# Optimization experiments

Hardware: AMD Instinct MI355X
Metric: run time of the kernel (lower is better)

The kernel has to match this reference:

```python
import jax, jax.numpy as jnp
import numpy as np

PAST = 15        # sum(num_classes[:-1])
NC = 20          # sum(num_classes)
ALPHA = 0.99
IGNORE = 255


def setup_inputs() -> dict:
    key = jax.random.key(0)
    k1, k2, k3, k4, k5, k6 = jax.random.split(key, 6)
    B, C, H, W = 8, NC, 512, 512
    logit = jax.random.normal(k1, (B, C, H, W), dtype=jnp.float32)
    # ema_prob is used as probabilities (gathered & compared to thresholds)
    ema_prob = jax.nn.softmax(jax.random.normal(k2, (B, C, H, W), dtype=jnp.float32), axis=1)
    ema_thresh = jax.random.uniform(k3, (NC,), dtype=jnp.float32, minval=0.2, maxval=0.8)
    real_labels = jax.random.randint(k4, (B, H, W), 0, NC, dtype=jnp.int64)
    # sprinkle ignore pixels (255) like real segmentation masks
    real_labels = jnp.where(jax.random.uniform(k5, (B, H, W)) < 0.1, IGNORE, real_labels)
    moving_prob_avg = jax.random.uniform(k6, (NC,), dtype=jnp.float32)
    return {"logit": logit, "ema_prob": ema_prob, "ema_thresh": ema_thresh,
            "real_labels": real_labels, "moving_prob_avg": moving_prob_avg}


def reference(logit, ema_prob, ema_thresh, real_labels, moving_prob_avg):
    # --- pseudo-labels from current model (detached softmax) ---
    logit_prob = jax.nn.softmax(jax.lax.stop_gradient(logit), axis=1)  # [B,C,H,W]
    labels = jnp.argmax(logit_prob[:, :PAST], axis=1)                   # [B,H,W]
    labels = jnp.where(real_labels >= PAST, real_labels, labels)
    idx = jnp.where(real_labels == IGNORE, 0, labels)
    scores = jnp.take_along_axis(logit_prob, idx[:, None], axis=1)[:, 0]  # [B,H,W]

    # --- per-class mean of scores + EMA update of moving_prob_avg ---
    flat_lab = labels.reshape(-1)
    flat_sc = scores.reshape(-1)
    seg = jnp.where(flat_lab == IGNORE, NC, flat_lab)  # route ignored to extra bucket
    sums = jax.ops.segment_sum(flat_sc, seg, num_segments=NC + 1)[:NC]
    counts = jax.ops.segment_sum(jnp.ones_like(flat_sc), seg, num_segments=NC + 1)[:NC]
    means = sums / jnp.maximum(counts, 1.0)
    mpa = moving_prob_avg  # numpy buffer in torch (no grad)
    new_mpa = jnp.where(counts > 0,
                        jnp.where(mpa == -1.0, means, (1.0 - ALPHA) * means + ALPHA * mpa),
                        mpa)

    # --- EMA-teacher pseudo labels + threshold mask ---
    ema_labels = jnp.argmax(ema_prob[:, :PAST], axis=1)
    ema_labels = jnp.where(real_labels >= PAST, real_labels, ema_labels)
    eidx = jnp.where(real_labels == IGNORE, 0, ema_labels)
    ema_scores = jnp.take_along_axis(ema_prob, eidx[:, None], axis=1)[:, 0]
    valid_cls = ema_labels < NC  # 255 never matches any class in the torch loop
    thr = ema_thresh[jnp.clip(ema_labels, 0, NC - 1)]
    ema_mask = valid_cls & (ema_scores >= thr)
    dynamic_labels = jnp.where(ema_mask, ema_labels, IGNORE)  # [B,H,W]

    # --- masked cross-entropy with per-class reweighting ---
    logp = jax.nn.log_softmax(logit, axis=1)
    cidx = jnp.clip(dynamic_labels, 0, NC - 1)
    losses = -jnp.take_along_axis(logp, cidx[:, None], axis=1)[:, 0]
    valid = dynamic_labels != IGNORE
    mult = jnp.where(valid, 1.0 - new_mpa[cidx], 1.0)
    losses = losses * jax.lax.stop_gradient(mult)  # multiplier is a host scalar in torch
    vs = valid.astype(losses.dtype)
    return jnp.sum(losses * vs) / jnp.sum(vs)
```

## Files before the change

kernel.cpp:

```cpp
#include <hip/hip_runtime.h>
#include <math.h>


#define PASTC 15
#define NCC   20
#define IGN   255
#define HW2   262144
#define ALPHAF 0.99f

__global__ __launch_bounds__(256, 6) void dl_main(
    const float* __restrict__ logit,
    const float* __restrict__ ema,
    const float* __restrict__ thresh,
    const int*   __restrict__ real,
    float*       __restrict__ ws)
{
    __shared__ float s_acc[61];
    __shared__ float s_thr[NCC];
    const int tid = threadIdx.x;
    if (tid < 61) s_acc[tid] = 0.0f;
    if (tid < NCC) s_thr[tid] = thresh[tid];
    __syncthreads();

    const int t  = blockIdx.x * 256 + tid;
    const int p0 = t << 1;
    const int b  = p0 >> 18;
    const int s  = p0 & (HW2 - 1);
    const size_t base = (((size_t)(b * NCC)) << 18) + (size_t)s;
    const float* eb = ema   + base;
    const float* lb = logit + base;

    const int2 rl2 = *reinterpret_cast<const int2*>(real + p0);
    const int rl[2] = {rl2.x, rl2.y};

    int   cap_ch[2];
    float se[2], x_m15[2], esel[2], xsel[2];
    int   arg15[2], earg[2];
#pragma unroll
    for (int j = 0; j < 2; ++j) {
        cap_ch[j] = (rl[j] == IGN) ? 0 : (rl[j] >= PASTC ? rl[j] : -1);
        se[j] = 0.0f; x_m15[j] = -INFINITY; esel[j] = -INFINITY;
        xsel[j] = 0.0f; arg15[j] = 0; earg[j] = 0;
    }

#pragma unroll
    for (int c = 0; c < NCC; ++c) {
        const float2 ve = *reinterpret_cast<const float2*>(eb + ((size_t)c << 18));
        const float2 vl = *reinterpret_cast<const float2*>(lb + ((size_t)c << 18));
        const float ev[2] = {ve.x, ve.y};
        const float xv[2] = {vl.x, vl.y};
#pragma unroll
        for (int j = 0; j < 2; ++j) {
            const float x = xv[j];
            se[j] += __expf(x);
            if (c < PASTC) {
                const bool gl = x > x_m15[j];
                x_m15[j] = gl ? x : x_m15[j];
                arg15[j] = gl ? c : arg15[j];
            }
            const bool upd = (cap_ch[j] < 0)
                               ? (c < PASTC && ev[j] > esel[j])
                               : (c == cap_ch[j]);
            esel[j] = upd ? ev[j] : esel[j];
            earg[j] = upd ? c    : earg[j];
            xsel[j] = upd ? x    : xsel[j];
        }
    }

    float vcnt = 0.0f;
#pragma unroll
    for (int j = 0; j < 2; ++j) {
        const float lse = __logf(se[j]);
        if (rl[j] != IGN) {
            const int   lab  = (rl[j] >= PASTC) ? rl[j] : arg15[j];
            const float sval = (rl[j] >= PASTC) ? xsel[j] : x_m15[j];
            const float prob = __expf(sval - lse);
            atomicAdd(&s_acc[lab], prob);
            atomicAdd(&s_acc[20 + lab], 1.0f);
        }
        const int  el    = (rl[j] >= PASTC) ? rl[j] : earg[j];
        const float th   = s_thr[el < NCC ? el : (NCC - 1)];
        const bool valid = (el < NCC) && (esel[j] >= th);
        if (valid) {
            atomicAdd(&s_acc[40 + el], lse - xsel[j]);
        }
        const unsigned long long bm = __ballot(valid);
        if ((tid & 63) == 0) vcnt += (float)__popcll(bm);
    }
    if ((tid & 63) == 0) atomicAdd(&s_acc[60], vcnt);

    __syncthreads();
    if (tid < 61) atomicAdd(&ws[tid], s_acc[tid]);
}

__global__ void dl_final(const float* __restrict__ ws,
                         const float* __restrict__ mpa,
                         float*       __restrict__ out)
{
    if (threadIdx.x == 0 && blockIdx.x == 0) {
        float acc = 0.0f;
        for (int c = 0; c < NCC; ++c) {
            const float ssum = ws[c];
            const float cnt  = ws[20 + c];
            const float lsum = ws[40 + c];
            const float m    = mpa[c];
            const float mean = ssum / fmaxf(cnt, 1.0f);
            const float nm   = (cnt > 0.0f)
                                 ? ((m == -1.0f) ? mean
                                                 : (1.0f - ALPHAF) * mean + ALPHAF * m)
                                 : m;
            acc += lsum * (1.0f - nm);
        }
        out[0] = acc / ws[60];
    }
}

extern "C" void kernel_launch(void* const* d_in, const int* in_sizes, int n_in,
                              void* d_out, int out_size, void* d_ws, size_t ws_size,
                              hipStream_t stream) {
    const float* logit  = (const float*)d_in[0];
    const float* ema    = (const float*)d_in[1];
    const float* thresh = (const float*)d_in[2];
    const int*   real   = (const int*)d_in[3];
    const float* mpa    = (const float*)d_in[4];
    float* out = (float*)d_out;
    float* ws  = (float*)d_ws;

    hipMemsetAsync(ws, 0, 64 * sizeof(float), stream);

    dl_main<<<4096, 256, 0, stream>>>(logit, ema, thresh, real, ws);
    dl_final<<<1, 64, 0, stream>>>(ws, mpa, out);
}
```

Baseline: 404.2 us.

## Process 16 pixels per thread with float4 loads and split ema/logit passes

Each thread now handles 16 pixels in four float4 groups instead of 2 pixels with float2 loads, and the grid shrinks from 4096 to 512 blocks. The channel loop is split into an ema pass, which finds the teacher label, followed by a logit pass that accumulates the softmax sum, the top-15 argmax and the selected logit. Both passes are specialised for the first 15 channels and the last 5. The aim is wider memory transactions, more loads in flight per thread and less per-block atomic and launch overhead, at the cost of higher register pressure, the removed launch bounds, and only 512 blocks to fill the device.

```diff
diff --git a/kernel.cpp b/kernel.cpp
--- a/kernel.cpp
+++ b/kernel.cpp
@@ -7,8 +7,10 @@
 #define IGN   255
 #define HW2   262144
 #define ALPHAF 0.99f
+#define PPT   16
+#define GRP   4
 
-__global__ __launch_bounds__(256, 6) void dl_main(
+__global__ void dl_main(
     const float* __restrict__ logit,
     const float* __restrict__ ema,
     const float* __restrict__ thresh,
@@ -22,54 +24,97 @@
     if (tid < NCC) s_thr[tid] = thresh[tid];
     __syncthreads();
 
-    const int t  = blockIdx.x * 256 + tid;
-    const int p0 = t << 1;
-    const int b  = p0 >> 18;
-    const int s  = p0 & (HW2 - 1);
-    const size_t base = (((size_t)(b * NCC)) << 18) + (size_t)s;
-    const float* eb = ema   + base;
-    const float* lb = logit + base;
+    const int P  = blockIdx.x * (256 * PPT);
+    const int b  = P >> 18;
+    const int sp = P & (HW2 - 1);
+    const size_t abase = (((size_t)(b * NCC)) << 18) + (size_t)sp;
+    const int lo = tid << 2;
 
-    const int2 rl2 = *reinterpret_cast<const int2*>(real + p0);
-    const int rl[2] = {rl2.x, rl2.y};
-
-    int   cap_ch[2];
-    float se[2], x_m15[2], esel[2], xsel[2];
-    int   arg15[2], earg[2];
+    int rl[PPT];
 #pragma unroll
-    for (int j = 0; j < 2; ++j) {
-        cap_ch[j] = (rl[j] == IGN) ? 0 : (rl[j] >= PASTC ? rl[j] : -1);
-        se[j] = 0.0f; x_m15[j] = -INFINITY; esel[j] = -INFINITY;
-        xsel[j] = 0.0f; arg15[j] = 0; earg[j] = 0;
+    for (int g = 0; g < GRP; ++g) {
+        const int4 r4 = *reinterpret_cast<const int4*>(real + P + g * 1024 + lo);
+        rl[g*4+0] = r4.x; rl[g*4+1] = r4.y; rl[g*4+2] = r4.z; rl[g*4+3] = r4.w;
     }
 
+    int   cap[PPT], earg[PPT];
+    float esel[PPT];
 #pragma unroll
-    for (int c = 0; c < NCC; ++c) {
-        const float2 ve = *reinterpret_cast<const float2*>(eb + ((size_t)c << 18));
-        const float2 vl = *reinterpret_cast<const float2*>(lb + ((size_t)c << 18));
-        const float ev[2] = {ve.x, ve.y};
-        const float xv[2] = {vl.x, vl.y};
+    for (int j = 0; j < PPT; ++j) {
+        cap[j]  = (rl[j] == IGN) ? 0 : (rl[j] >= PASTC ? rl[j] : -1);
+        esel[j] = -INFINITY; earg[j] = 0;
+    }
+
+    const float* eb = ema + abase;
+#pragma unroll 3
+    for (int c = 0; c < PASTC; ++c) {
+        float4 v[GRP];
 #pragma unroll
-        for (int j = 0; j < 2; ++j) {
-            const float x = xv[j];
+        for (int g = 0; g < GRP; ++g)
+            v[g] = *reinterpret_cast<const float4*>(eb + ((size_t)c << 18) + g * 1024 + lo);
+#pragma unroll
+        for (int j = 0; j < PPT; ++j) {
+            const float ev = ((const float*)&v[j >> 2])[j & 3];
+            const bool upd = (cap[j] < 0) ? (ev > esel[j]) : (c == cap[j]);
+            esel[j] = upd ? ev : esel[j];
+            earg[j] = upd ? c  : earg[j];
+        }
+    }
+#pragma unroll 1
+    for (int c = PASTC; c < NCC; ++c) {
+        float4 v[GRP];
+#pragma unroll
+        for (int g = 0; g < GRP; ++g)
+            v[g] = *reinterpret_cast<const float4*>(eb + ((size_t)c << 18) + g * 1024 + lo);
+#pragma unroll
+        for (int j = 0; j < PPT; ++j) {
+            const float ev = ((const float*)&v[j >> 2])[j & 3];
+            const bool upd = (c == cap[j]);
+            esel[j] = upd ? ev : esel[j];
+            earg[j] = upd ? c  : earg[j];
+        }
+    }
+
+    float se[PPT], x_m15[PPT], xsel[PPT];
+    int   arg15[PPT];
+#pragma unroll
+    for (int j = 0; j < PPT; ++j) {
+        se[j] = 0.0f; x_m15[j] = -INFINITY; xsel[j] = 0.0f; arg15[j] = 0;
+    }
+    const float* lb = logit + abase;
+#pragma unroll 3
+    for (int c = 0; c < PASTC; ++c) {
+        float4 v[GRP];
+#pragma unroll
+        for (int g = 0; g < GRP; ++g)
+            v[g] = *reinterpret_cast<const float4*>(lb + ((size_t)c << 18) + g * 1024 + lo);
+#pragma unroll
+        for (int j = 0; j < PPT; ++j) {
+            const float x = ((const float*)&v[j >> 2])[j & 3];
             se[j] += __expf(x);
-            if (c < PASTC) {
-                const bool gl = x > x_m15[j];
-                x_m15[j] = gl ? x : x_m15[j];
-                arg15[j] = gl ? c : arg15[j];
-            }
-            const bool upd = (cap_ch[j] < 0)
-                               ? (c < PASTC && ev[j] > esel[j])
-                               : (c == cap_ch[j]);
-            esel[j] = upd ? ev[j] : esel[j];
-            earg[j] = upd ? c    : earg[j];
-            xsel[j] = upd ? x    : xsel[j];
+            const bool gl = x > x_m15[j];
+            x_m15[j] = gl ? x : x_m15[j];
+            arg15[j] = gl ? c : arg15[j];
+            xsel[j]  = (c == earg[j]) ? x : xsel[j];
+        }
+    }
+#pragma unroll 1
+    for (int c = PASTC; c < NCC; ++c) {
+        float4 v[GRP];
+#pragma unroll
+        for (int g = 0; g < GRP; ++g)
+            v[g] = *reinterpret_cast<const float4*>(lb + ((size_t)c << 18) + g * 1024 + lo);
+#pragma unroll
+        for (int j = 0; j < PPT; ++j) {
+            const float x = ((const float*)&v[j >> 2])[j & 3];
+            se[j] += __expf(x);
+            xsel[j] = (c == earg[j]) ? x : xsel[j];
         }
     }
 
     float vcnt = 0.0f;
 #pragma unroll
-    for (int j = 0; j < 2; ++j) {
+    for (int j = 0; j < PPT; ++j) {
         const float lse = __logf(se[j]);
         if (rl[j] != IGN) {
             const int   lab  = (rl[j] >= PASTC) ? rl[j] : arg15[j];
@@ -128,6 +173,6 @@
 
     hipMemsetAsync(ws, 0, 64 * sizeof(float), stream);
 
-    dl_main<<<4096, 256, 0, stream>>>(logit, ema, thresh, real, ws);
+    dl_main<<<512, 256, 0, stream>>>(logit, ema, thresh, real, ws);
     dl_final<<<1, 64, 0, stream>>>(ws, mpa, out);
 }
```

Result: faster. 382.3 us (-5.4%).
